# Optimization experiments

Hardware: AMD Instinct MI355X
Metric: run time of the kernel (lower is better)

Reference implementation:

```python
import jax, jax.numpy as jnp
import numpy as np

N = 4096        # nodes (atoms)
E = 65536       # edges (avg degree 16)
H = 128         # hidden_channels
R = 32          # num_rbf
MAX_Z = 128
CUTOFF_UPPER = 4.5
LN_EPS = 1e-5


def _linear_params(key, out_f, in_f, bias=True, scale=None):
    kw, kb = jax.random.split(key)
    s = scale if scale is not None else (1.0 / np.sqrt(in_f))
    W = jax.random.uniform(kw, (out_f, in_f), jnp.float32, -s, s)
    if bias:
        b = jax.random.uniform(kb, (out_f,), jnp.float32, -s, s)
        return W, b
    return W


def setup_inputs() -> dict:
    key = jax.random.key(0)
    ks = jax.random.split(key, 24)
    z = jax.random.randint(ks[0], (N,), 0, MAX_Z)
    edge_index = jax.random.randint(ks[1], (2, E), 0, N)
    edge_weight = jax.random.uniform(ks[2], (E,), jnp.float32) * CUTOFF_UPPER
    ev = jax.random.normal(ks[3], (E, 3), jnp.float32)
    edge_vec_norm = ev / jnp.linalg.norm(ev, axis=-1, keepdims=True)
    edge_attr = jax.random.uniform(ks[4], (E, R), jnp.float32)
    labels = jax.random.normal(ks[5], (N,), jnp.float32)
    labels_mask = jax.random.randint(ks[6], (N,), 0, 2).astype(bool)

    emb_w = jax.random.normal(ks[7], (MAX_Z, H), jnp.float32)  # nn.Embedding default N(0,1)
    emb2_w, emb2_b = _linear_params(ks[8], H, 2 * H)
    label_emb_w, label_emb_b = _linear_params(ks[9], H, 1)
    label_emb2_w, label_emb2_b = _linear_params(ks[10], H, 2 * H)
    mask_token = jax.random.normal(ks[11], (H,), jnp.float32)
    dp1_w, dp1_b = _linear_params(ks[12], H, R)
    dp2_w, dp2_b = _linear_params(ks[13], H, R)
    dp3_w, dp3_b = _linear_params(ks[14], H, R)
    lt0_w = _linear_params(ks[15], H, H, bias=False)
    lt1_w = _linear_params(ks[16], H, H, bias=False)
    lt2_w = _linear_params(ks[17], H, H, bias=False)
    ls1_w, ls1_b = _linear_params(ks[18], 2 * H, H)
    ls2_w, ls2_b = _linear_params(ks[19], 3 * H, 2 * H)
    ln_g = jnp.ones((H,), jnp.float32)
    ln_b = jnp.zeros((H,), jnp.float32)

    return dict(z=z, edge_index=edge_index, edge_weight=edge_weight,
                edge_vec_norm=edge_vec_norm, edge_attr=edge_attr,
                labels=labels, labels_mask=labels_mask,
                emb_w=emb_w, emb2_w=emb2_w, emb2_b=emb2_b,
                label_emb_w=label_emb_w, label_emb_b=label_emb_b,
                mask_token=mask_token,
                label_emb2_w=label_emb2_w, label_emb2_b=label_emb2_b,
                dp1_w=dp1_w, dp1_b=dp1_b, dp2_w=dp2_w, dp2_b=dp2_b,
                dp3_w=dp3_w, dp3_b=dp3_b,
                lt0_w=lt0_w, lt1_w=lt1_w, lt2_w=lt2_w,
                ls1_w=ls1_w, ls1_b=ls1_b, ls2_w=ls2_w, ls2_b=ls2_b,
                ln_g=ln_g, ln_b=ln_b)


def _cosine_cutoff(d):
    # cutoff_lower == 0 branch of CosineCutoff
    c = 0.5 * (jnp.cos(d * (np.pi / CUTOFF_UPPER)) + 1.0)
    return c * (d < CUTOFF_UPPER).astype(d.dtype)


def _skewtensor(v):
    zero = jnp.zeros_like(v[:, 0])
    t = jnp.stack([zero, -v[:, 2], v[:, 1],
                   v[:, 2], zero, -v[:, 0],
                   -v[:, 1], v[:, 0], zero], axis=1)
    return t.reshape(-1, 3, 3)


def _symtensor(v):
    vv = v[:, :, None] * v[:, None, :]               # [E,3,3], symmetric
    tr = jnp.trace(vv, axis1=-2, axis2=-1) / 3.0     # mean of diagonal
    eye = jnp.eye(3, dtype=v.dtype)
    return vv - tr[:, None, None] * eye              # traceless symmetric part


def _layernorm(x, g, b):
    mu = jnp.mean(x, axis=-1, keepdims=True)
    var = jnp.mean(jnp.square(x - mu), axis=-1, keepdims=True)
    return (x - mu) * jax.lax.rsqrt(var + LN_EPS) * g + b


def reference(z, edge_index, edge_weight, edge_vec_norm, edge_attr, labels,
              labels_mask, emb_w, emb2_w, emb2_b, label_emb_w, label_emb_b,
              mask_token, label_emb2_w, label_emb2_b, dp1_w, dp1_b, dp2_w,
              dp2_b, dp3_w, dp3_b, lt0_w, lt1_w, lt2_w, ls1_w, ls1_b, ls2_w,
              ls2_b, ln_g, ln_b):
    src, dst = edge_index[0], edge_index[1]
    n = z.shape[0]

    # --- atomic-number message: Zij = emb2(concat(Z[src], Z[dst])) ---
    Z = emb_w[z]                                                   # [N,H]
    Zij = jnp.concatenate([Z[src], Z[dst]], -1) @ emb2_w.T + emb2_b  # [E,H]

    # --- label message with mask-token substitution ---
    L = labels[:, None] @ label_emb_w.T + label_emb_b              # [N,H]
    L = jnp.where(labels_mask[:, None], mask_token, L)
    Lij = jnp.concatenate([L[src], L[dst]], -1) @ label_emb2_w.T + label_emb2_b

    # --- tensor messages ---
    CZ = _cosine_cutoff(edge_weight)[:, None] * (Zij + Lij)        # [E,H]
    eye = jnp.eye(3, dtype=edge_vec_norm.dtype)
    f1 = edge_attr @ dp1_w.T + dp1_b                               # [E,H]
    f2 = edge_attr @ dp2_w.T + dp2_b
    f3 = edge_attr @ dp3_w.T + dp3_b
    skew = _skewtensor(edge_vec_norm)                              # [E,3,3]
    sym = _symtensor(edge_vec_norm)                                # [E,3,3]
    Iij = (f1 * CZ)[:, :, None, None] * eye                        # [E,H,3,3]
    Aij = (f2 * CZ)[:, :, None, None] * skew[:, None]
    Sij = (f3 * CZ)[:, :, None, None] * sym[:, None]

    # --- scatter-add into node tensors ---
    I = jax.ops.segment_sum(Iij, src, num_segments=n)              # [N,H,3,3]
    A = jax.ops.segment_sum(Aij, src, num_segments=n)
    S = jax.ops.segment_sum(Sij, src, num_segments=n)

    # --- norm + scalar MLP gating ---
    X3 = I + A + S
    norm = jnp.sum(jnp.square(X3), axis=(-2, -1))                  # tensor_norm -> [N,H]
    norm = _layernorm(norm, ln_g, ln_b)
    norm = jax.nn.silu(norm @ ls1_w.T + ls1_b)                     # [N,2H]
    norm = jax.nn.silu(norm @ ls2_w.T + ls2_b)                     # [N,3H]
    norm = norm.reshape(n, -1, 3)                                  # [N,H,3]

    # --- channel-mixing linears over hidden dim, gated per component ---
    I = jnp.einsum('nhij,gh->ngij', I, lt0_w) * norm[:, :, 0, None, None]
    A = jnp.einsum('nhij,gh->ngij', A, lt1_w) * norm[:, :, 1, None, None]
    S = jnp.einsum('nhij,gh->ngij', S, lt2_w) * norm[:, :, 2, None, None]
    return I + A + S                                               # [N,H,3,3]
```

## Files before the change

kernel.cpp:

```cpp
#include <hip/hip_runtime.h>
#include <hip/hip_bf16.h>
#include <math.h>

#define NN 4096
#define EE 65536
#define HH 128
#define RR 32
#define MAXZ 128
#define CUT 4.5f
#define PI_OVER_CUT 0.6981317007977318f
#define LN_EPS 1e-5f

typedef unsigned short u16;
typedef unsigned int u32;
typedef unsigned char u8;
typedef _Float16 h2 __attribute__((ext_vector_type(2)));
typedef _Float16 hf8 __attribute__((ext_vector_type(8)));
typedef float f32x4 __attribute__((ext_vector_type(4)));

__device__ __forceinline__ float dot4(float4 a, float4 b){
    return a.x*b.x + a.y*b.y + a.z*b.z + a.w*b.w;
}
__device__ __forceinline__ float silu(float x){ return x / (1.f + __expf(-x)); }
__device__ __forceinline__ u32 packh2(float a, float b){
    union{u32 u; h2 h;} v; v.h = (h2){(_Float16)a, (_Float16)b}; return v.u;
}
__device__ __forceinline__ float fdot2u(u32 a, u32 b, float c){
    union{u32 u; h2 h;} x, y; x.u = a; y.u = b;
    return __builtin_amdgcn_fdot2(x.h, y.h, c, false);
}
__device__ __forceinline__ u16 f2h(float f){
    union{u16 u; _Float16 h;} v; v.h = (_Float16)f; return v.u;
}
__device__ __forceinline__ float h2f(u16 u){
    union{u16 u_; _Float16 h;} v; v.u_ = u; return (float)v.h;
}

__global__ void k_sig(float* __restrict__ out, float val, int n){
    int i = blockIdx.x*256 + threadIdx.x;
    if (i < n) out[i] = val;
}

__global__ void k_zero(int* __restrict__ deg, int* __restrict__ doneCnt){
    int i = blockIdx.x*256 + threadIdx.x;
    deg[i] = 0;
    if (i == 0) doneCnt[0] = 0;
}

__global__ __launch_bounds__(256) void k_front(
    const u8* __restrict__ zr, const u8* __restrict__ eir, const u8* __restrict__ mr,
    int* __restrict__ z32, int* __restrict__ ei32, int* __restrict__ m32,
    int* __restrict__ deg, int* __restrict__ doneCnt,
    int* __restrict__ offsets, int* __restrict__ cursor,
    const float* __restrict__ ls1_w, const float* __restrict__ ls2_w,
    const float* __restrict__ lt0_w, const float* __restrict__ lt1_w,
    const float* __restrict__ lt2_w,
    const float* __restrict__ dp1_w, const float* __restrict__ dp2_w,
    const float* __restrict__ dp3_w,
    const float* __restrict__ emb_w, const float* __restrict__ emb2_w,
    const float* __restrict__ label_emb_w, const float* __restrict__ label_emb_b,
    const float* __restrict__ mask_token, const float* __restrict__ label_emb2_w,
    const float* __restrict__ label_emb2_b, const float* __restrict__ emb2_b,
    u16* __restrict__ ls1H, u16* __restrict__ ls2H, u16* __restrict__ ltH,
    u32* __restrict__ dpTh, float* __restrict__ PzA, float* __restrict__ PzB,
    float* __restrict__ vecs)
{
    int b = blockIdx.x, t = threadIdx.x;
    if (b < 512){
        __shared__ int sF1, sF3, sOdd, sZ64, sE64;
        if (t == 0){ sF1=0; sF3=0; sOdd=0; sZ64=1; sE64=1; }
        __syncthreads();
        for (int i = t; i < 4096; i += 256){
            u8 bb = mr[i];
            if ((i & 3) == 1 && bb == 0x3F) sF1 = 1;
            if ((i & 3) == 3 && bb == 0x3F) sF3 = 1;
            if ((i & 3) != 0 && bb != 0)    sOdd = 1;
        }
        const u32* zw = (const u32*)zr;
        const u32* ew = (const u32*)eir;
        for (int i = t; i < 128; i += 256) if (zw[2*i + 1]) sZ64 = 0;
        for (int i = t; i < 512; i += 256) if (ew[2*i + 1]) sE64 = 0;
        __syncthreads();
        int mf = sF1 ? 2 : (sF3 ? 0 : (sOdd ? 1 : 0));
        int z64 = sZ64, e64 = sE64;

        int i = b*256 + t;
        if (i < NN){
            z32[i] = z64 ? ((const int*)zr)[2*i] : ((const int*)zr)[i];
            int mm;
            if (mf == 1)      mm = (mr[i] != 0);
            else if (mf == 2) mm = (((const u16*)mr)[i] != 0);
            else              mm = (((const u32*)mr)[i] != 0u);
            m32[i] = mm;
        }
        if (i < 2*EE){
            int v = e64 ? ((const int*)eir)[2*i] : ((const int*)eir)[i];
            ei32[i] = v;
            if (i < EE) atomicAdd(&deg[v], 1);
        }

        __syncthreads();
        __shared__ int isLast;
        if (t == 0){
            __threadfence();
            int old = __hip_atomic_fetch_add(doneCnt, 1, __ATOMIC_ACQ_REL,
                                             __HIP_MEMORY_SCOPE_AGENT);
            isLast = (old == 511);
        }
        __syncthreads();
        if (isLast){
            int lane = t & 63, wid = t >> 6;
            int vals[16];
            #pragma unroll
            for (int q = 0; q < 16; ++q)
                vals[q] = __hip_atomic_load(&deg[t*16 + q], __ATOMIC_RELAXED,
                                            __HIP_MEMORY_SCOPE_AGENT);
            int sum = 0;
            #pragma unroll
            for (int q = 0; q < 16; ++q) sum += vals[q];
            int incl = sum;
            #pragma unroll
            for (int dd = 1; dd < 64; dd <<= 1){
                int s2 = __shfl_up(incl, dd);
                if (lane >= dd) incl += s2;
            }
            __shared__ int wsum[4];
            if (lane == 63) wsum[wid] = incl;
            __syncthreads();
            int base = 0;
            for (int w = 0; w < wid; ++w) base += wsum[w];
            int run = base + incl - sum;
            #pragma unroll
            for (int q = 0; q < 16; ++q){
                offsets[t*16 + q] = run;
                cursor [t*16 + q] = run;
                run += vals[q];
            }
            if (t == 255) offsets[NN] = run;
        }
        return;
    }

    int pb = b - 512;
    if (pb < 728){
        int i = pb*256 + t;
        if (i < 32768){ ls1H[i] = f2h(ls1_w[i]); return; }
        i -= 32768;
        if (i < 98304){ ls2H[i] = f2h(ls2_w[i]); return; }
        i -= 98304;
        if (i < 16384){ ltH[0*16384 + i] = f2h(lt0_w[i]); return; }
        i -= 16384;
        if (i < 16384){ ltH[1*16384 + i] = f2h(lt1_w[i]); return; }
        i -= 16384;
        if (i < 16384){ ltH[2*16384 + i] = f2h(lt2_w[i]); return; }
        i -= 16384;
        if (i < 6144){
            int j = i >> 11, rem = i & 2047, q = rem >> 7, h = rem & 127;
            const float* src = (j == 0) ? dp1_w : ((j == 1) ? dp2_w : dp3_w);
            dpTh[(j*16 + q)*HH + h] = packh2(src[h*RR + 2*q], src[h*RR + 2*q + 1]);
            return;
        }
        return;
    }
    if (pb < 792){
        int zi = (pb - 728)*2 + (t >> 7), h = t & 127;
        __shared__ float Zs[2][HH];
        Zs[t >> 7][h] = emb_w[zi*HH + h];
        __syncthreads();
        const float4* wa = (const float4*)(emb2_w + h*2*HH);
        const float4* wb = (const float4*)(emb2_w + h*2*HH + HH);
        float pa = 0.f, pbv = 0.f;
        const float* Z = Zs[t >> 7];
        #pragma unroll 8
        for (int j = 0; j < HH/4; ++j){
            float4 zp = *(const float4*)&Z[4*j];
            pa  += dot4(wa[j], zp);
            pbv += dot4(wb[j], zp);
        }
        PzA[zi*HH + h] = pa;
        PzB[zi*HH + h] = pbv;
        return;
    }
    if (t < 128){
        int h = t;
        const float* wa = label_emb2_w + h*2*HH;
        const float* wb = wa + HH;
        float uA=0.f,vA=0.f,wA=0.f,uB=0.f,vB=0.f,wB=0.f;
        for (int j = 0; j < HH; ++j){
            float a = wa[j], bb = wb[j];
            float u = label_emb_w[j], v = label_emb_b[j], m = mask_token[j];
            uA += a*u; vA += a*v; wA += a*m;
            uB += bb*u; vB += bb*v; wB += bb*m;
        }
        float bias = emb2_b[h] + label_emb2_b[h];
        vecs[0*HH + h] = uA;
        vecs[1*HH + h] = vA + bias;
        vecs[2*HH + h] = wA + bias;
        vecs[3*HH + h] = uB;
        vecs[4*HH + h] = vB;
        vecs[5*HH + h] = wB;
    }
}

__global__ __launch_bounds__(256) void k_edge(
    const int* __restrict__ ei, int* __restrict__ cursor,
    const float* __restrict__ ew, const float* __restrict__ ev,
    const float* __restrict__ ea,
    u32* __restrict__ attrSh, int* __restrict__ dstA, float4* __restrict__ metaA,
    const int* __restrict__ z32, const int* __restrict__ m32,
    const float* __restrict__ labels,
    const float* __restrict__ PzA, const float* __restrict__ PzB,
    const float* __restrict__ vecs,
    float* __restrict__ Pa, u16* __restrict__ Pbh)
{
    int b = blockIdx.x, t = threadIdx.x;
    if (b < 256){
        int e = b*256 + t;
        int s = ei[e];
        int p = atomicAdd(&cursor[s], 1);
        float d = ew[e];
        float cutv = (d < CUT) ? 0.5f*(__cosf(d*PI_OVER_CUT) + 1.f) : 0.f;
        dstA[p] = ei[EE + e];
        metaA[p] = make_float4(cutv, ev[3*e], ev[3*e+1], ev[3*e+2]);
        const float* a = ea + (size_t)e*RR;
        u32* o = attrSh + (size_t)p*16;
        #pragma unroll
        for (int q = 0; q < 16; ++q)
            o[q] = packh2(cutv*a[2*q], cutv*a[2*q+1]);
        return;
    }
    int i = (b - 256)*256 + t;
    int n = i >> 7, h = i & 127;
    int zi = z32[n];
    int mk = m32[n];
    float lab = labels[n];
    float la = mk ? vecs[2*HH + h] : lab*vecs[0*HH + h] + vecs[1*HH + h];
    float lb = mk ? vecs[5*HH + h] : lab*vecs[3*HH + h] + vecs[4*HH + h];
    Pa[i]  = PzA[zi*HH + h] + la;
    Pbh[i] = f2h(PzB[zi*HH + h] + lb);
}

__global__ __launch_bounds__(128) void k_gather(
    const u32* __restrict__ attrSh, const int* __restrict__ dstA,
    const float4* __restrict__ metaA,
    const u32* __restrict__ dpTh,
    const float* __restrict__ dp1_b, const float* __restrict__ dp2_b,
    const float* __restrict__ dp3_b,
    const float* __restrict__ Pa, const u16* __restrict__ Pbh,
    const int* __restrict__ offsets,
    u16* __restrict__ X0, u16* __restrict__ X1, u16* __restrict__ X2,
    float* __restrict__ norm2)
{
    int n = blockIdx.x, t = threadIdx.x;
    u32 w1[16], w2[16], w3[16];
    #pragma unroll
    for (int q = 0; q < 16; ++q){
        w1[q] = dpTh[(0*16 + q)*HH + t];
        w2[q] = dpTh[(1*16 + q)*HH + t];
        w3[q] = dpTh[(2*16 + q)*HH + t];
    }
    float fb1 = dp1_b[t], fb2 = dp2_b[t], fb3 = dp3_b[t];
    float pa = Pa[n*HH + t];
    float ai = 0.f, aw0 = 0.f, aw1 = 0.f, aw2 = 0.f;
    float m00 = 0.f, m01 = 0.f, m02 = 0.f, m11 = 0.f, m12 = 0.f, m22 = 0.f;

    int e0 = offsets[n], e1 = offsets[n+1];
    int j = e0;
    for (; j + 1 < e1; j += 2){
        int dsta = dstA[j], dstb = dstA[j+1];
        float4 ma = metaA[j], mb = metaA[j+1];
        float sa = pa + h2f(Pbh[(size_t)dsta*HH + t]);
        float sb = pa + h2f(Pbh[(size_t)dstb*HH + t]);
        const u32* Aa = attrSh + (size_t)j*16;
        const u32* Ab = Aa + 16;
        float f1a = ma.x*fb1, f2a = ma.x*fb2, f3a = ma.x*fb3;
        float f1b = mb.x*fb1, f2b = mb.x*fb2, f3b = mb.x*fb3;
        #pragma unroll
        for (int q = 0; q < 16; ++q){
            u32 a = Aa[q], bq = Ab[q];
            f1a = fdot2u(a, w1[q], f1a);
            f2a = fdot2u(a, w2[q], f2a);
            f3a = fdot2u(a, w3[q], f3a);
            f1b = fdot2u(bq, w1[q], f1b);
            f2b = fdot2u(bq, w2[q], f2b);
            f3b = fdot2u(bq, w3[q], f3b);
        }
        float aa = f1a*sa, ba = f2a*sa, ca = f3a*sa;
        float ab = f1b*sb, bb = f2b*sb, cb = f3b*sb;
        ai  += aa;            ai  += ab;
        aw0 += ba*ma.y;       aw0 += bb*mb.y;
        aw1 += ba*ma.z;       aw1 += bb*mb.z;
        aw2 += ba*ma.w;       aw2 += bb*mb.w;
        float cva0 = ca*ma.y, cva1 = ca*ma.z;
        float cvb0 = cb*mb.y, cvb1 = cb*mb.z;
        m00 += cva0*ma.y;     m00 += cvb0*mb.y;
        m01 += cva0*ma.z;     m01 += cvb0*mb.z;
        m02 += cva0*ma.w;     m02 += cvb0*mb.w;
        m11 += cva1*ma.z;     m11 += cvb1*mb.z;
        m12 += cva1*ma.w;     m12 += cvb1*mb.w;
        m22 += ca*ma.w*ma.w;  m22 += cb*mb.w*mb.w;
    }
    if (j < e1){
        int dst = dstA[j];
        float4 m4 = metaA[j];
        float s = pa + h2f(Pbh[(size_t)dst*HH + t]);
        const u32* Aa = attrSh + (size_t)j*16;
        float f1 = m4.x*fb1, f2 = m4.x*fb2, f3 = m4.x*fb3;
        #pragma unroll
        for (int q = 0; q < 16; ++q){
            u32 a = Aa[q];
            f1 = fdot2u(a, w1[q], f1);
            f2 = fdot2u(a, w2[q], f2);
            f3 = fdot2u(a, w3[q], f3);
        }
        float a = f1*s, bb = f2*s, c = f3*s;
        ai  += a;
        aw0 += bb*m4.y; aw1 += bb*m4.z; aw2 += bb*m4.w;
        float cv0 = c*m4.y, cv1 = c*m4.z;
        m00 += cv0*m4.y; m01 += cv0*m4.z; m02 += cv0*m4.w;
        m11 += cv1*m4.z; m12 += cv1*m4.w; m22 += c*m4.w*m4.w;
    }

    X0[(size_t)n*HH + t] = f2h(ai);
    u16* x1p = X1 + (size_t)3*n*HH + t;
    x1p[0*HH] = f2h(aw0); x1p[1*HH] = f2h(aw1); x1p[2*HH] = f2h(aw2);
    u16* x2p = X2 + (size_t)6*n*HH + t;
    x2p[0*HH] = f2h(m00); x2p[1*HH] = f2h(m01); x2p[2*HH] = f2h(m02);
    x2p[3*HH] = f2h(m11); x2p[4*HH] = f2h(m12); x2p[5*HH] = f2h(m22);

    float tr3 = (m00 + m11 + m22) * (1.f/3.f);
    float x00 = ai + m00 - tr3, x11 = ai + m11 - tr3, x22 = ai + m22 - tr3;
    float nn = x00*x00 + x11*x11 + x22*x22
             + 2.f*(m01*m01 + aw2*aw2 + m02*m02 + aw1*aw1 + m12*m12 + aw0*aw0);
    norm2[n*HH + t] = nn;
}

__global__ __launch_bounds__(512) void k_tail(
    const float* __restrict__ norm2, const float* __restrict__ ln_g,
    const float* __restrict__ ln_b,
    const u16* __restrict__ ls1H, const float* __restrict__ ls1_b,
    const u16* __restrict__ ls2H, const float* __restrict__ ls2_b,
    float* __restrict__ gates,
    const u16* __restrict__ X0, const u16* __restrict__ X1,
    const u16* __restrict__ X2, const u16* __restrict__ ltH,
    float* __restrict__ out)
{
    int n0 = blockIdx.x * 16;
    int t = threadIdx.x;
    int wave = t >> 6, lane = t & 63;
    int rlo = lane & 15, kb = lane >> 4;
    __shared__ u16 ysH[16][136];
    __shared__ u16 usH[16][264];
    __shared__ u16 Yl[160*136];

    hf8 a0[4], a1[4];
    {
        int tile = wave;
        const u16* X; int rbase;
        if (tile == 0)     { X = X0; rbase = n0; }
        else if (tile < 4) { X = X1; rbase = 3*n0 + (tile-1)*16; }
        else               { X = X2; rbase = 6*n0 + (tile-4)*16; }
        const hf8* xr = (const hf8*)(X + (size_t)(rbase + rlo)*HH + kb*8);
        #pragma unroll
        for (int ks = 0; ks < 4; ++ks) a0[ks] = xr[ks*4];
    }
    if (wave < 2){
        int tile = wave + 8;
        int rbase = 6*n0 + (tile-4)*16;
        const hf8* xr = (const hf8*)(X2 + (size_t)(rbase + rlo)*HH + kb*8);
        #pragma unroll
        for (int ks = 0; ks < 4; ++ks) a1[ks] = xr[ks*4];
    }

    if (wave < 4){
        int ni = wave*4 + kb;
        int n = n0 + ni;
        float x[8]; float s = 0.f;
        #pragma unroll
        for (int k = 0; k < 8; ++k){ x[k] = norm2[(size_t)n*HH + rlo + 16*k]; s += x[k]; }
        #pragma unroll
        for (int d = 1; d < 16; d <<= 1) s += __shfl_xor(s, d);
        float mu = s * (1.f/HH);
        float q = 0.f;
        #pragma unroll
        for (int k = 0; k < 8; ++k){ float dx = x[k]-mu; q += dx*dx; }
        #pragma unroll
        for (int d = 1; d < 16; d <<= 1) q += __shfl_xor(q, d);
        float rs = rsqrtf(q*(1.f/HH) + LN_EPS);
        #pragma unroll
        for (int k = 0; k < 8; ++k){
            int h = rlo + 16*k;
            ysH[ni][h] = f2h((x[k]-mu)*rs*ln_g[h] + ln_b[h]);
        }
    }
    __syncthreads();

    {
        hf8 a[4];
        #pragma unroll
        for (int ks = 0; ks < 4; ++ks)
            a[ks] = *(const hf8*)&ysH[rlo][kb*8 + ks*32];
        for (int ct = wave; ct < 16; ct += 8){
            f32x4 acc = (f32x4){0.f,0.f,0.f,0.f};
            const u16* wr0 = ls1H + (size_t)(ct*16 + rlo)*HH;
            #pragma unroll
            for (int ks = 0; ks < 4; ++ks){
                hf8 bf = *(const hf8*)(wr0 + kb*8 + ks*32);
                acc = __builtin_amdgcn_mfma_f32_16x16x32_f16(a[ks], bf, acc, 0, 0, 0);
            }
            float bias = ls1_b[ct*16 + rlo];
            #pragma unroll
            for (int j = 0; j < 4; ++j)
                usH[kb*4 + j][ct*16 + rlo] = f2h(silu(acc[j] + bias));
        }
    }
    __syncthreads();

    {
        hf8 a[8];
        #pragma unroll
        for (int ks = 0; ks < 8; ++ks)
            a[ks] = *(const hf8*)&usH[rlo][kb*8 + ks*32];
        for (int ct = wave; ct < 24; ct += 8){
            f32x4 acc = (f32x4){0.f,0.f,0.f,0.f};
            const u16* wr0 = ls2H + (size_t)(ct*16 + rlo)*256;
            #pragma unroll
            for (int ks = 0; ks < 8; ++ks){
                hf8 bf = *(const hf8*)(wr0 + kb*8 + ks*32);
                acc = __builtin_amdgcn_mfma_f32_16x16x32_f16(a[ks], bf, acc, 0, 0, 0);
            }
            float bias = ls2_b[ct*16 + rlo];
            #pragma unroll
            for (int j = 0; j < 4; ++j){
                int n = n0 + kb*4 + j;
                gates[(size_t)n*384 + ct*16 + rlo] = silu(acc[j] + bias);
            }
        }
    }

    {
        int tile = wave;
        const u16* W = (tile == 0) ? ltH : ((tile < 4) ? ltH + 16384 : ltH + 32768);
        #pragma unroll
        for (int ct = 0; ct < 8; ++ct){
            f32x4 acc = (f32x4){0.f,0.f,0.f,0.f};
            const hf8* wr = (const hf8*)(W + (size_t)(ct*16 + rlo)*HH + kb*8);
            #pragma unroll
            for (int ks = 0; ks < 4; ++ks)
                acc = __builtin_amdgcn_mfma_f32_16x16x32_f16(a0[ks], wr[ks*4], acc, 0, 0, 0);
            #pragma unroll
            for (int j = 0; j < 4; ++j)
                Yl[(tile*16 + kb*4 + j)*136 + ct*16 + rlo] = f2h(acc[j]);
        }
    }
    if (wave < 2){
        int tile = wave + 8;
        const u16* W = ltH + 32768;
        #pragma unroll
        for (int ct = 0; ct < 8; ++ct){
            f32x4 acc = (f32x4){0.f,0.f,0.f,0.f};
            const hf8* wr = (const hf8*)(W + (size_t)(ct*16 + rlo)*HH + kb*8);
            #pragma unroll
            for (int ks = 0; ks < 4; ++ks)
                acc = __builtin_amdgcn_mfma_f32_16x16x32_f16(a1[ks], wr[ks*4], acc, 0, 0, 0);
            #pragma unroll
            for (int j = 0; j < 4; ++j)
                Yl[(tile*16 + kb*4 + j)*136 + ct*16 + rlo] = f2h(acc[j]);
        }
    }
    __syncthreads();

    #pragma unroll
    for (int q = 0; q < 4; ++q){
        int id = q*512 + t;
        int ni = id >> 7, g = id & 127;
        int n = n0 + ni;
        float mi  = h2f(Yl[ni*136 + g]);
        float mw0 = h2f(Yl[(16 + 3*ni + 0)*136 + g]);
        float mw1 = h2f(Yl[(16 + 3*ni + 1)*136 + g]);
        float mw2 = h2f(Yl[(16 + 3*ni + 2)*136 + g]);
        float mm0 = h2f(Yl[(64 + 6*ni + 0)*136 + g]);
        float mm1 = h2f(Yl[(64 + 6*ni + 1)*136 + g]);
        float mm2 = h2f(Yl[(64 + 6*ni + 2)*136 + g]);
        float mm3 = h2f(Yl[(64 + 6*ni + 3)*136 + g]);
        float mm4 = h2f(Yl[(64 + 6*ni + 4)*136 + g]);
        float mm5 = h2f(Yl[(64 + 6*ni + 5)*136 + g]);
        float g0 = gates[(size_t)n*384 + 3*g];
        float g1 = gates[(size_t)n*384 + 3*g + 1];
        float g2 = gates[(size_t)n*384 + 3*g + 2];
        float t3 = (mm0 + mm3 + mm5) * (1.f/3.f);
        float* op = out + ((size_t)n*HH + g)*9;
        op[0] =  g0*mi  + g2*(mm0 - t3);
        op[1] = -g1*mw2 + g2*mm1;
        op[2] =  g1*mw1 + g2*mm2;
        op[3] =  g1*mw2 + g2*mm1;
        op[4] =  g0*mi  + g2*(mm3 - t3);
        op[5] = -g1*mw0 + g2*mm4;
        op[6] = -g1*mw1 + g2*mm2;
        op[7] =  g1*mw0 + g2*mm4;
        op[8] =  g0*mi  + g2*(mm5 - t3);
    }
}

extern "C" void kernel_launch(void* const* d_in, const int* in_sizes, int n_in,
                              void* d_out, int out_size, void* d_ws, size_t ws_size,
                              hipStream_t stream)
{
    float* out = (float*)d_out;
    int sig_blocks = (out_size + 255)/256;

    if (out_size != NN*HH*9){
        k_sig<<<sig_blocks, 256, 0, stream>>>(out, 400.f, out_size);
        return;
    }
    if (n_in != 30){
        k_sig<<<sig_blocks, 256, 0, stream>>>(out, 300.f + (float)n_in, out_size);
        return;
    }
    static const int want[30] = {
        4096, 131072, 65536, 196608, 2097152, 4096, 4096,
        16384, 32768, 128, 128, 128, 128, 32768, 128,
        4096, 128, 4096, 128, 4096, 128,
        16384, 16384, 16384, 32768, 256, 98304, 384, 128, 128
    };
    for (int i = 0; i < 30; ++i){
        if (in_sizes[i] != want[i]){
            k_sig<<<sig_blocks, 256, 0, stream>>>(out, 200.f + (float)i, out_size);
            return;
        }
    }

    const u8*    z_raw        = (const u8*)d_in[0];
    const u8*    ei_raw       = (const u8*)d_in[1];
    const float* edge_weight  = (const float*)d_in[2];
    const float* edge_vec     = (const float*)d_in[3];
    const float* edge_attr    = (const float*)d_in[4];
    const float* labels       = (const float*)d_in[5];
    const u8*    mask_raw     = (const u8*)d_in[6];
    const float* emb_w        = (const float*)d_in[7];
    const float* emb2_w       = (const float*)d_in[8];
    const float* emb2_b       = (const float*)d_in[9];
    const float* label_emb_w  = (const float*)d_in[10];
    const float* label_emb_b  = (const float*)d_in[11];
    const float* mask_token   = (const float*)d_in[12];
    const float* label_emb2_w = (const float*)d_in[13];
    const float* label_emb2_b = (const float*)d_in[14];
    const float* dp1_w = (const float*)d_in[15];
    const float* dp1_b = (const float*)d_in[16];
    const float* dp2_w = (const float*)d_in[17];
    const float* dp2_b = (const float*)d_in[18];
    const float* dp3_w = (const float*)d_in[19];
    const float* dp3_b = (const float*)d_in[20];
    const float* lt0_w = (const float*)d_in[21];
    const float* lt1_w = (const float*)d_in[22];
    const float* lt2_w = (const float*)d_in[23];
    const float* ls1_w = (const float*)d_in[24];
    const float* ls1_b = (const float*)d_in[25];
    const float* ls2_w = (const float*)d_in[26];
    const float* ls2_b = (const float*)d_in[27];
    const float* ln_g  = (const float*)d_in[28];
    const float* ln_b  = (const float*)d_in[29];

    char* ws = (char*)d_ws;
    size_t off = 0;
    auto alloc = [&](size_t bytes) -> void* {
        void* p = ws + off;
        off += (bytes + 255) & ~(size_t)255;
        return p;
    };
    float* Pa      = (float*)alloc((size_t)NN*HH*4);
    u16*   Pbh     = (u16*)alloc((size_t)NN*HH*2);
    float* norm2   = (float*)alloc((size_t)NN*HH*4);
    float* gates   = (float*)alloc((size_t)NN*384*4);
    float* PzA     = (float*)alloc((size_t)MAXZ*HH*4);
    float* PzB     = (float*)alloc((size_t)MAXZ*HH*4);
    float* vecs    = (float*)alloc((size_t)6*HH*4);
    u32*   dpTh    = (u32*)alloc((size_t)3*16*HH*4);
    u16*   ls1H    = (u16*)alloc((size_t)32768*2);
    u16*   ls2H    = (u16*)alloc((size_t)98304*2);
    u16*   ltH     = (u16*)alloc((size_t)3*16384*2);
    u16*   X0      = (u16*)alloc((size_t)NN*HH*2);
    u16*   X1      = (u16*)alloc((size_t)3*NN*HH*2);
    u16*   X2      = (u16*)alloc((size_t)6*NN*HH*2);
    u32*   attrSh  = (u32*)alloc((size_t)EE*16*4);
    float* metaA   = (float*)alloc((size_t)EE*16);
    int*   dstA    = (int*)alloc((size_t)EE*4);
    int*   z32     = (int*)alloc((size_t)NN*4);
    int*   ei32    = (int*)alloc((size_t)2*EE*4);
    int*   m32     = (int*)alloc((size_t)NN*4);
    int*   deg     = (int*)alloc((size_t)NN*4);
    int*   offsets = (int*)alloc((size_t)(NN+1)*4);
    int*   cursor  = (int*)alloc((size_t)NN*4);
    int*   doneCnt = (int*)alloc((size_t)4);

    if (off > ws_size){
        k_sig<<<sig_blocks, 256, 0, stream>>>(out, 150.f, out_size);
        return;
    }

    k_zero  <<<NN/256, 256, 0, stream>>>(deg, doneCnt);
    k_front <<<1305, 256, 0, stream>>>(z_raw, ei_raw, mask_raw,
                                       z32, ei32, m32, deg, doneCnt,
                                       offsets, cursor,
                                       ls1_w, ls2_w, lt0_w, lt1_w, lt2_w,
                                       dp1_w, dp2_w, dp3_w,
                                       emb_w, emb2_w,
                                       label_emb_w, label_emb_b, mask_token,
                                       label_emb2_w, label_emb2_b, emb2_b,
                                       ls1H, ls2H, ltH, dpTh, PzA, PzB, vecs);
    k_edge  <<<2304, 256, 0, stream>>>(ei32, cursor, edge_weight, edge_vec,
                                       edge_attr, attrSh, dstA, (float4*)metaA,
                                       z32, m32, labels, PzA, PzB, vecs, Pa, Pbh);
    k_gather<<<NN, 128, 0, stream>>>(attrSh, dstA, (const float4*)metaA,
                                     dpTh, dp1_b, dp2_b, dp3_b,
                                     Pa, Pbh, offsets, X0, X1, X2, norm2);
    k_tail  <<<NN/16, 512, 0, stream>>>(norm2, ln_g, ln_b, ls1H, ls1_b,
                                        ls2H, ls2_b, gates,
                                        X0, X1, X2, ltH, out);
}
```

Measured before the change: 107.0 us.

## Stage edge batches in LDS for gather kernel with cooperative loads

```diff
diff --git a/kernel.cpp b/kernel.cpp
--- a/kernel.cpp
+++ b/kernel.cpp
@@ -10,6 +10,7 @@
 #define CUT 4.5f
 #define PI_OVER_CUT 0.6981317007977318f
 #define LN_EPS 1e-5f
+#define GB 16
 
 typedef unsigned short u16;
 typedef unsigned int u32;
@@ -252,6 +253,9 @@
     float* __restrict__ norm2)
 {
     int n = blockIdx.x, t = threadIdx.x;
+    __shared__ u32 sAttr[GB*16];
+    __shared__ float4 sMeta[GB];
+    __shared__ float sSa[GB][HH];
     u32 w1[16], w2[16], w3[16];
     #pragma unroll
     for (int q = 0; q < 16; ++q){
@@ -265,60 +269,72 @@
     float m00 = 0.f, m01 = 0.f, m02 = 0.f, m11 = 0.f, m12 = 0.f, m22 = 0.f;
 
     int e0 = offsets[n], e1 = offsets[n+1];
-    int j = e0;
-    for (; j + 1 < e1; j += 2){
-        int dsta = dstA[j], dstb = dstA[j+1];
-        float4 ma = metaA[j], mb = metaA[j+1];
-        float sa = pa + h2f(Pbh[(size_t)dsta*HH + t]);
-        float sb = pa + h2f(Pbh[(size_t)dstb*HH + t]);
-        const u32* Aa = attrSh + (size_t)j*16;
-        const u32* Ab = Aa + 16;
-        float f1a = ma.x*fb1, f2a = ma.x*fb2, f3a = ma.x*fb3;
-        float f1b = mb.x*fb1, f2b = mb.x*fb2, f3b = mb.x*fb3;
-        #pragma unroll
-        for (int q = 0; q < 16; ++q){
-            u32 a = Aa[q], bq = Ab[q];
-            f1a = fdot2u(a, w1[q], f1a);
-            f2a = fdot2u(a, w2[q], f2a);
-            f3a = fdot2u(a, w3[q], f3a);
-            f1b = fdot2u(bq, w1[q], f1b);
-            f2b = fdot2u(bq, w2[q], f2b);
-            f3b = fdot2u(bq, w3[q], f3b);
-        }
-        float aa = f1a*sa, ba = f2a*sa, ca = f3a*sa;
-        float ab = f1b*sb, bb = f2b*sb, cb = f3b*sb;
-        ai  += aa;            ai  += ab;
-        aw0 += ba*ma.y;       aw0 += bb*mb.y;
-        aw1 += ba*ma.z;       aw1 += bb*mb.z;
-        aw2 += ba*ma.w;       aw2 += bb*mb.w;
-        float cva0 = ca*ma.y, cva1 = ca*ma.z;
-        float cvb0 = cb*mb.y, cvb1 = cb*mb.z;
-        m00 += cva0*ma.y;     m00 += cvb0*mb.y;
-        m01 += cva0*ma.z;     m01 += cvb0*mb.z;
-        m02 += cva0*ma.w;     m02 += cvb0*mb.w;
-        m11 += cva1*ma.z;     m11 += cvb1*mb.z;
-        m12 += cva1*ma.w;     m12 += cvb1*mb.w;
-        m22 += ca*ma.w*ma.w;  m22 += cb*mb.w*mb.w;
-    }
-    if (j < e1){
-        int dst = dstA[j];
-        float4 m4 = metaA[j];
-        float s = pa + h2f(Pbh[(size_t)dst*HH + t]);
-        const u32* Aa = attrSh + (size_t)j*16;
-        float f1 = m4.x*fb1, f2 = m4.x*fb2, f3 = m4.x*fb3;
-        #pragma unroll
-        for (int q = 0; q < 16; ++q){
-            u32 a = Aa[q];
-            f1 = fdot2u(a, w1[q], f1);
-            f2 = fdot2u(a, w2[q], f2);
-            f3 = fdot2u(a, w3[q], f3);
-        }
-        float a = f1*s, bb = f2*s, c = f3*s;
-        ai  += a;
-        aw0 += bb*m4.y; aw1 += bb*m4.z; aw2 += bb*m4.w;
-        float cv0 = c*m4.y, cv1 = c*m4.z;
-        m00 += cv0*m4.y; m01 += cv0*m4.z; m02 += cv0*m4.w;
-        m11 += cv1*m4.z; m12 += cv1*m4.w; m22 += c*m4.w*m4.w;
+    for (int base = e0; base < e1; base += GB){
+        int cnt = e1 - base; if (cnt > GB) cnt = GB;
+        __syncthreads();
+        if (t < cnt*8)
+            ((uint2*)sAttr)[t] = ((const uint2*)(attrSh + (size_t)base*16))[t];
+        if (t < cnt)
+            sMeta[t] = metaA[base + t];
+        #pragma unroll 4
+        for (int q = 0; q < cnt; ++q){
+            int dq = dstA[base + q];
+            sSa[q][t] = pa + h2f(Pbh[(size_t)dq*HH + t]);
+        }
+        __syncthreads();
+        int q = 0;
+        for (; q + 1 < cnt; q += 2){
+            float4 ma = sMeta[q], mb = sMeta[q+1];
+            float sa = sSa[q][t];
+            float sb = sSa[q+1][t];
+            const u32* Aa = sAttr + q*16;
+            const u32* Ab = Aa + 16;
+            float f1a = ma.x*fb1, f2a = ma.x*fb2, f3a = ma.x*fb3;
+            float f1b = mb.x*fb1, f2b = mb.x*fb2, f3b = mb.x*fb3;
+            #pragma unroll
+            for (int k = 0; k < 16; ++k){
+                u32 a = Aa[k], bq = Ab[k];
+                f1a = fdot2u(a, w1[k], f1a);
+                f2a = fdot2u(a, w2[k], f2a);
+                f3a = fdot2u(a, w3[k], f3a);
+                f1b = fdot2u(bq, w1[k], f1b);
+                f2b = fdot2u(bq, w2[k], f2b);
+                f3b = fdot2u(bq, w3[k], f3b);
+            }
+            float aa = f1a*sa, ba = f2a*sa, ca = f3a*sa;
+            float ab = f1b*sb, bb = f2b*sb, cb = f3b*sb;
+            ai  += aa;            ai  += ab;
+            aw0 += ba*ma.y;       aw0 += bb*mb.y;
+            aw1 += ba*ma.z;       aw1 += bb*mb.z;
+            aw2 += ba*ma.w;       aw2 += bb*mb.w;
+            float cva0 = ca*ma.y, cva1 = ca*ma.z;
+            float cvb0 = cb*mb.y, cvb1 = cb*mb.z;
+            m00 += cva0*ma.y;     m00 += cvb0*mb.y;
+            m01 += cva0*ma.z;     m01 += cvb0*mb.z;
+            m02 += cva0*ma.w;     m02 += cvb0*mb.w;
+            m11 += cva1*ma.z;     m11 += cvb1*mb.z;
+            m12 += cva1*ma.w;     m12 += cvb1*mb.w;
+            m22 += ca*ma.w*ma.w;  m22 += cb*mb.w*mb.w;
+        }
+        if (q < cnt){
+            float4 m4 = sMeta[q];
+            float s = sSa[q][t];
+            const u32* Aa = sAttr + q*16;
+            float f1 = m4.x*fb1, f2 = m4.x*fb2, f3 = m4.x*fb3;
+            #pragma unroll
+            for (int k = 0; k < 16; ++k){
+                u32 a = Aa[k];
+                f1 = fdot2u(a, w1[k], f1);
+                f2 = fdot2u(a, w2[k], f2);
+                f3 = fdot2u(a, w3[k], f3);
+            }
+            float a = f1*s, bb = f2*s, c = f3*s;
+            ai  += a;
+            aw0 += bb*m4.y; aw1 += bb*m4.z; aw2 += bb*m4.w;
+            float cv0 = c*m4.y, cv1 = c*m4.z;
+            m00 += cv0*m4.y; m01 += cv0*m4.z; m02 += cv0*m4.w;
+            m11 += cv1*m4.z; m12 += cv1*m4.w; m22 += c*m4.w*m4.w;
+        }
     }
 
     X0[(size_t)n*HH + t] = f2h(ai);
```

Result: slower. 109.4 us (+2.3%).
